# Kernel optimization log

Measured on AMD Instinct MI355X. Metric: run time of the kernel, lower is better.

Reference implementation:

```python
import jax, jax.numpy as jnp
import numpy as np

E = 16      # num_experts
K = 2       # top-k
C = 1280    # capacity = ceil(8192*2/16*1.25)


def setup_inputs() -> dict:
    key = jax.random.key(0)
    ks = jax.random.split(key, 7)
    B, T, D, F, DFF = 4, 2048, 1024, 512, 512
    s = 0.02
    return {
        "hidden_state": jax.random.normal(ks[0], (B, T, D), jnp.float32),
        "router_w": jax.random.normal(ks[1], (D, E), jnp.float32) * s,
        "shared_gate_w": jax.random.normal(ks[2], (D, 1), jnp.float32) * s,
        "w1": jax.random.normal(ks[3], (E, D, F), jnp.float32) * s,
        "w2": jax.random.normal(ks[4], (E, F, D), jnp.float32) * s,
        "sw1": jax.random.normal(ks[5], (D, DFF), jnp.float32) * s,
        "sw2": jax.random.normal(ks[6], (DFF, D), jnp.float32) * s,
    }


def reference(hidden_state, router_w, shared_gate_w, w1, w2, sw1, sw2):
    B, T, D = hidden_state.shape
    N = B * T
    # Router: softmax over expert logits + shared sigmoid gate
    logits = jnp.einsum("btd,de->bte", hidden_state, router_w)
    scores = jax.nn.softmax(logits, axis=-1)                      # [B,T,E]
    g_shared = jax.nn.sigmoid(jnp.einsum("btd,do->bto", hidden_state, shared_gate_w))

    topk_vals, topk_idx = jax.lax.top_k(scores, K)                # [B,T,K]
    x = hidden_state.reshape(N, D)
    token_for_route = jnp.repeat(jnp.arange(N), K)                # [N*K]
    expert_for_route = topk_idx.reshape(-1)                       # [N*K]
    gate_for_route = topk_vals.reshape(-1)                        # [N*K]

    # Stable sort by expert (jnp.argsort is stable)
    order = jnp.argsort(expert_for_route)
    expert_sorted = expert_for_route[order]
    token_sorted = token_for_route[order]
    gate_sorted = gate_for_route[order]
    x_sorted = x[token_sorted]                                    # [N*K, D]

    counts = jnp.bincount(expert_sorted, length=E)
    starts = jnp.cumsum(counts) - counts
    r = jnp.arange(N * K)
    positions = r - starts[expert_sorted]                         # slot within expert
    keep = (positions < C) & (gate_sorted != 0)
    p_idx = jnp.clip(positions, 0, C - 1)

    # Scatter kept tokens into fixed-capacity buffers; dropped routes go to dummy row E
    e_safe = jnp.where(keep, expert_sorted, E)
    p_safe = jnp.where(keep, p_idx, 0)
    buf = jnp.zeros((E + 1, C, D), x.dtype).at[e_safe, p_safe].set(
        jnp.where(keep[:, None], x_sorted, 0.0)
    )
    expert_inputs = buf[:E]                                       # [E,C,D]

    # Batched expert FFN (exact GELU, matching torch default)
    h = jax.nn.gelu(jnp.einsum("ech,ehf->ecf", expert_inputs, w1), approximate=False)
    expert_outputs = jnp.einsum("ecf,efh->ech", h, w2)            # [E,C,D]

    gate_eff = jnp.where(keep, gate_sorted, 0.0)
    y_sorted = expert_outputs[expert_sorted, p_idx] * gate_eff[:, None]

    # Combine: scatter-add back to tokens
    y_out = jnp.zeros((N, D), x.dtype).at[token_sorted].add(y_sorted).reshape(B, T, D)

    # Shared expert path
    shared_out = (jax.nn.gelu(x @ sw1, approximate=False) @ sw2).reshape(B, T, D)
    y_out = y_out + g_shared * shared_out

    # Stats (no attention_mask path)
    load_counts = jnp.bincount(expert_for_route, length=E)
    load = load_counts / (load_counts.sum() + 1e-12)
    importance = scores.mean(axis=(0, 1))
    return (y_out, importance, load)
```

## Files before the change

kernel.cpp:

```cpp
#include <hip/hip_runtime.h>
#include <hip/hip_bf16.h>
#include <math.h>

#define N_TOK 8192
#define DIM 1024
#define NEXP 16
#define CAP 1280
#define FDIM 512
#define NROUTE (N_TOK * 2)
#define NCHUNK 64
#define ECAP (NEXP * CAP)
#define TOTROW (ECAP + N_TOK)

typedef __hip_bfloat16 bf16;
typedef unsigned short ushort_t;
typedef __attribute__((ext_vector_type(8))) short bf16x8;
typedef __attribute__((ext_vector_type(4))) float f32x4;

__device__ __forceinline__ float gelu_fast(float x) {
    float u = 1.5957691216057308f * (x + 0.044715f * x * x * x);
    return x / (1.f + __expf(-u));
}

__device__ __forceinline__ float bf2f(unsigned short u) {
    union { float f; unsigned int i; } v; v.i = ((unsigned int)u) << 16; return v.f;
}

__device__ __forceinline__ unsigned short f2b(float f) {
    union { __hip_bfloat16 h; unsigned short u; } v;
    v.h = __float2bfloat16(f);
    return v.u;
}

__device__ __forceinline__ void gload16(const void* g, void* l) {
    __builtin_amdgcn_global_load_lds(
        (const __attribute__((address_space(1))) unsigned int*)g,
        (__attribute__((address_space(3))) unsigned int*)l,
        16, 0, 0);
}

__device__ __forceinline__ int swz_addr16(int r, int q) {
    return ((r >> 1) << 3) + ((r & 1) << 2) + (q ^ ((r >> 1) & 3));
}

__global__ __launch_bounds__(256) void gather_x_kernel(
    const ushort_t* __restrict__ x_bf, const int* __restrict__ slot_token,
    const int* __restrict__ counts_cap, ushort_t* __restrict__ xg)
{
    int row = blockIdx.x;
    int e = row / CAP;
    int pos = row - e * CAP;
    int tok = (pos < counts_cap[e]) ? slot_token[row] : 0;
    if ((unsigned)tok >= N_TOK) tok = 0;
    int c = threadIdx.x * 4;
    ushort4 v = *reinterpret_cast<const ushort4*>(x_bf + (size_t)tok * DIM + c);
    *reinterpret_cast<ushort4*>(xg + (size_t)row * DIM + c) = v;
}

#define PREP_RTR_BLOCKS 1024
#define PREP_NWG (PREP_RTR_BLOCKS + 1088)
__global__ __launch_bounds__(256) void prep_kernel(
    const float* __restrict__ x, const float* __restrict__ rw,
    const float* __restrict__ sgw,
    const float* __restrict__ w1, const float* __restrict__ w2,
    const float* __restrict__ sw1, const float* __restrict__ sw2,
    float* __restrict__ scores,
    int* __restrict__ topk_idx,
    float* __restrict__ topk_val,
    float* __restrict__ g_shared,
    ushort_t* __restrict__ x_bf,
    ushort_t* __restrict__ w1t, ushort_t* __restrict__ w2t,
    ushort_t* __restrict__ sw1t, ushort_t* __restrict__ sw2t)
{
    __shared__ union {
        ushort_t tileB[128][130];
        struct {
            float xl[8][1028];
            float racc[4][8][4][4];
            float g[4][8];
        } r;
    } sm;

    if (blockIdx.x < PREP_RTR_BLOCKS) {
        int tid = threadIdx.x;
        int w = tid >> 6;
        int lane = tid & 63;
        int tok0 = blockIdx.x * 8;

        {
            int dq = w * 256 + lane * 4;
            float4 gv = *reinterpret_cast<const float4*>(sgw + dq);
#pragma unroll
            for (int tt = 0; tt < 8; ++tt) {
                const float* xr = x + (size_t)(tok0 + tt) * DIM + dq;
                float4 xv = *reinterpret_cast<const float4*>(xr);
                *reinterpret_cast<float4*>(&sm.r.xl[tt][dq]) = xv;
                ushort4 o;
                o.x = f2b(xv.x); o.y = f2b(xv.y); o.z = f2b(xv.z); o.w = f2b(xv.w);
                *reinterpret_cast<ushort4*>(x_bf + (size_t)(tok0 + tt) * DIM + dq) = o;
                float dg = xv.x * gv.x + xv.y * gv.y + xv.z * gv.z + xv.w * gv.w;
#pragma unroll
                for (int m = 1; m < 64; m <<= 1) dg += __shfl_xor(dg, m, 64);
                if (lane == 0) sm.r.g[w][tt] = dg;
            }
        }
        __syncthreads();

        int tok = lane >> 3;
        int dup = (lane >> 2) & 1;
        int e4 = lane & 3;
        {
            int base_d = w * 256 + dup * 128;
            const float* rwb = rw + (size_t)base_d * NEXP + e4 * 4;
            float4 a0 = {0,0,0,0}, a1 = {0,0,0,0}, a2 = {0,0,0,0}, a3 = {0,0,0,0};
#pragma unroll 4
            for (int i = 0; i < 32; ++i) {
                float4 xv = *reinterpret_cast<const float4*>(&sm.r.xl[tok][base_d + i * 4]);
                const float* rp = rwb + (size_t)i * 4 * NEXP;
                float4 w0 = *reinterpret_cast<const float4*>(rp);
                float4 w1v = *reinterpret_cast<const float4*>(rp + NEXP);
                float4 w2v = *reinterpret_cast<const float4*>(rp + 2 * NEXP);
                float4 w3v = *reinterpret_cast<const float4*>(rp + 3 * NEXP);
                a0.x += xv.x * w0.x;  a0.y += xv.x * w0.y;  a0.z += xv.x * w0.z;  a0.w += xv.x * w0.w;
                a1.x += xv.y * w1v.x; a1.y += xv.y * w1v.y; a1.z += xv.y * w1v.z; a1.w += xv.y * w1v.w;
                a2.x += xv.z * w2v.x; a2.y += xv.z * w2v.y; a2.z += xv.z * w2v.z; a2.w += xv.z * w2v.w;
                a3.x += xv.w * w3v.x; a3.y += xv.w * w3v.y; a3.z += xv.w * w3v.z; a3.w += xv.w * w3v.w;
            }
            float s0 = (a0.x + a1.x) + (a2.x + a3.x);
            float s1 = (a0.y + a1.y) + (a2.y + a3.y);
            float s2 = (a0.z + a1.z) + (a2.z + a3.z);
            float s3 = (a0.w + a1.w) + (a2.w + a3.w);
            s0 += __shfl_xor(s0, 4, 64);
            s1 += __shfl_xor(s1, 4, 64);
            s2 += __shfl_xor(s2, 4, 64);
            s3 += __shfl_xor(s3, 4, 64);
            if (dup == 0) {
                sm.r.racc[w][tok][e4][0] = s0;
                sm.r.racc[w][tok][e4][1] = s1;
                sm.r.racc[w][tok][e4][2] = s2;
                sm.r.racc[w][tok][e4][3] = s3;
            }
        }
        __syncthreads();

        if (tid >= 32) return;
        int tk = tid >> 2;
        int eq = tid & 3;
        int token = tok0 + tk;
        float L0 = sm.r.racc[0][tk][eq][0] + sm.r.racc[1][tk][eq][0]
                 + sm.r.racc[2][tk][eq][0] + sm.r.racc[3][tk][eq][0];
        float L1 = sm.r.racc[0][tk][eq][1] + sm.r.racc[1][tk][eq][1]
                 + sm.r.racc[2][tk][eq][1] + sm.r.racc[3][tk][eq][1];
        float L2 = sm.r.racc[0][tk][eq][2] + sm.r.racc[1][tk][eq][2]
                 + sm.r.racc[2][tk][eq][2] + sm.r.racc[3][tk][eq][2];
        float L3 = sm.r.racc[0][tk][eq][3] + sm.r.racc[1][tk][eq][3]
                 + sm.r.racc[2][tk][eq][3] + sm.r.racc[3][tk][eq][3];

        float mx = fmaxf(fmaxf(L0, L1), fmaxf(L2, L3));
        mx = fmaxf(mx, __shfl_xor(mx, 1, 4));
        mx = fmaxf(mx, __shfl_xor(mx, 2, 4));
        float P0 = expf(L0 - mx), P1 = expf(L1 - mx);
        float P2 = expf(L2 - mx), P3 = expf(L3 - mx);
        float s = (P0 + P1) + (P2 + P3);
        s += __shfl_xor(s, 1, 4);
        s += __shfl_xor(s, 2, 4);
        float inv = 1.f / s;
        P0 *= inv; P1 *= inv; P2 *= inv; P3 *= inv;

        float4 Pv = {P0, P1, P2, P3};
        *reinterpret_cast<float4*>(scores + (size_t)token * NEXP + eq * 4) = Pv;

        int base = eq * 4;
        float v = P0; int idx = base;
        if (P1 > v) { v = P1; idx = base + 1; }
        if (P2 > v) { v = P2; idx = base + 2; }
        if (P3 > v) { v = P3; idx = base + 3; }
#pragma unroll
        for (int m = 1; m < 4; m <<= 1) {
            float vo = __shfl_xor(v, m, 4);
            int io = __shfl_xor(idx, m, 4);
            if (vo > v || (vo == v && io < idx)) { v = vo; idx = io; }
        }
        int i0 = idx; float v0 = v;
        float q0 = (base + 0 == i0) ? -1.f : P0;
        float q1 = (base + 1 == i0) ? -1.f : P1;
        float q2 = (base + 2 == i0) ? -1.f : P2;
        float q3 = (base + 3 == i0) ? -1.f : P3;
        v = q0; idx = base;
        if (q1 > v) { v = q1; idx = base + 1; }
        if (q2 > v) { v = q2; idx = base + 2; }
        if (q3 > v) { v = q3; idx = base + 3; }
#pragma unroll
        for (int m = 1; m < 4; m <<= 1) {
            float vo = __shfl_xor(v, m, 4);
            int io = __shfl_xor(idx, m, 4);
            if (vo > v || (vo == v && io < idx)) { v = vo; idx = io; }
        }
        if (eq == 0) {
            topk_idx[2 * token] = i0; topk_idx[2 * token + 1] = idx;
            topk_val[2 * token] = v0; topk_val[2 * token + 1] = v;
            float ag = (sm.r.g[0][tk] + sm.r.g[1][tk]) + (sm.r.g[2][tk] + sm.r.g[3][tk]);
            g_shared[token] = 1.f / (1.f + expf(-ag));
        }
        return;
    }

    int bx = blockIdx.x - PREP_RTR_BLOCKS;
    const float* src; ushort_t* dst; int K, N, kt, nt;
    if (bx < 512) {
        int e = bx >> 5, r = bx & 31;
        K = 1024; N = 512; kt = r >> 2; nt = r & 3;
        src = w1 + (size_t)e * K * N; dst = w1t + (size_t)e * K * N;
    } else if (bx < 1024) {
        int b2 = bx - 512, e = b2 >> 5, r = b2 & 31;
        K = 512; N = 1024; kt = r >> 3; nt = r & 7;
        src = w2 + (size_t)e * K * N; dst = w2t + (size_t)e * K * N;
    } else if (bx < 1056) {
        int r = bx - 1024;
        K = 1024; N = 512; kt = r >> 2; nt = r & 3;
        src = sw1; dst = sw1t;
    } else {
        int r = bx - 1056;
        K = 512; N = 1024; kt = r >> 3; nt = r & 7;
        src = sw2; dst = sw2t;
    }
    int t = threadIdx.x;
#pragma unroll 4
    for (int i = 0; i < 16; ++i) {
        int u = t + 256 * i;
        int r = u >> 5;
        int c4 = (u & 31) * 4;
        float4 v = *reinterpret_cast<const float4*>(
            src + (size_t)(kt * 128 + r) * N + nt * 128 + c4);
        sm.tileB[c4 + 0][r] = f2b(v.x);
        sm.tileB[c4 + 1][r] = f2b(v.y);
        sm.tileB[c4 + 2][r] = f2b(v.z);
        sm.tileB[c4 + 3][r] = f2b(v.w);
    }
    __syncthreads();
#pragma unroll 4
    for (int i2 = 0; i2 < 8; ++i2) {
        int u = t + 256 * i2;
        int n = u >> 4;
        int kc = (u & 15) * 8;
        bf16x8 o;
#pragma unroll
        for (int j = 0; j < 8; ++j) o[j] = (short)sm.tileB[n][kc + j];
        *reinterpret_cast<bf16x8*>(dst + (size_t)(nt * 128 + n) * K + kt * 128 + kc) = o;
    }
}

__global__ __launch_bounds__(256) void hist_kernel(
    const int* __restrict__ topk_idx, int* __restrict__ chunk_hist)
{
    __shared__ int h[NEXP];
    int tid = threadIdx.x;
    if (tid < NEXP) h[tid] = 0;
    __syncthreads();
    int r = blockIdx.x * 256 + tid;
    atomicAdd(&h[topk_idx[r]], 1);
    __syncthreads();
    if (tid < NEXP) chunk_hist[blockIdx.x * NEXP + tid] = h[tid];
}

__global__ __launch_bounds__(64) void scan_kernel(
    const int* __restrict__ chunk_hist, int* __restrict__ chunk_off,
    int* __restrict__ counts_cap, float* __restrict__ out_tail)
{
    int e = threadIdx.x;
    if (e >= NEXP) return;
    int run = 0;
    for (int b = 0; b < NCHUNK; ++b) {
        chunk_off[b * NEXP + e] = run;
        run += chunk_hist[b * NEXP + e];
    }
    counts_cap[e] = run < CAP ? run : CAP;
    out_tail[NEXP + e] = (float)((double)run / 16384.0);
}

__global__ __launch_bounds__(256) void assign_kernel(
    const int* __restrict__ topk_idx, const float* __restrict__ topk_val,
    const int* __restrict__ chunk_off,
    int* __restrict__ route_slot, int* __restrict__ slot_token)
{
    __shared__ int wave_cnt[4][NEXP];
    int tid = threadIdx.x;
    int lane = tid & 63;
    int w = tid >> 6;
    int r = blockIdx.x * 256 + tid;
    int e = topk_idx[r];
    float gate = topk_val[r];
    int rank_w = 0;
#pragma unroll
    for (int e16 = 0; e16 < NEXP; ++e16) {
        unsigned long long bal = __ballot(e == e16);
        if (e == e16) rank_w = __popcll(bal & ((1ull << lane) - 1ull));
        if (lane == 0) wave_cnt[w][e16] = __popcll(bal);
    }
    __syncthreads();
    int rank = rank_w;
#pragma unroll
    for (int w2 = 0; w2 < 3; ++w2)
        if (w2 < w) rank += wave_cnt[w2][e];
    int pos = chunk_off[blockIdx.x * NEXP + e] + rank;
    int slot = -1;
    if (pos < CAP && gate != 0.f) {
        slot = e * CAP + pos;
        slot_token[slot] = r >> 1;
    }
    route_slot[r] = slot;
}

__global__ __launch_bounds__(256) void importance_kernel(
    const float* __restrict__ scores, float* __restrict__ out_tail)
{
    __shared__ float red[256];
    int e = blockIdx.x;
    float s = 0.f;
    for (int t = threadIdx.x; t < N_TOK; t += 256) s += scores[t * NEXP + e];
    red[threadIdx.x] = s;
    __syncthreads();
    for (int st = 128; st > 0; st >>= 1) {
        if (threadIdx.x < st) red[threadIdx.x] += red[threadIdx.x + st];
        __syncthreads();
    }
    if (threadIdx.x == 0) out_tail[e] = red[0] / (float)N_TOK;
}

#define G1_GX (NEXP * 5 + N_TOK / 256)
#define G1_NWG (G1_GX * (FDIM / 128))
__global__ __launch_bounds__(512) void gemm1_mfma(
    const ushort_t* __restrict__ xg,
    const ushort_t* __restrict__ x_bf,
    const ushort_t* __restrict__ w1t,
    const ushort_t* __restrict__ sw1t,
    const int* __restrict__ counts_cap,
    ushort_t* __restrict__ h_buf)
{
    __shared__ ushort_t As[3][256 * 32];
    __shared__ ushort_t Bs[3][128 * 32];

    int flat = blockIdx.x;
    int wg = (flat & 7) * (G1_NWG / 8) + (flat >> 3);
    int by = wg & 3;
    int bxg = wg >> 2;

    int g, rb;
    if (bxg < NEXP * 5) { g = bxg / 5; rb = bxg % 5; }
    else { g = NEXP; rb = bxg - NEXP * 5; }
    int Mg = (g < NEXP) ? counts_cap[g] : N_TOK;
    int m0 = rb * 256;
    if (m0 >= Mg) return;
    const ushort_t* Arows = (g < NEXP) ? (xg + ((size_t)g * CAP + m0) * DIM)
                                       : (x_bf + (size_t)m0 * DIM);
    const ushort_t* Bt = (g < NEXP) ? (w1t + (size_t)g * DIM * FDIM) : sw1t;
    int n0 = by * 128;
    int t = threadIdx.x;

    const ushort_t* asrc[2];
    const ushort_t* bsrc;
#pragma unroll
    for (int i = 0; i < 2; ++i) {
        int s = t + i * 512;
        int lr = ((s >> 3) << 1) | ((s >> 2) & 1);
        int qq = (s & 3) ^ ((s >> 3) & 3);
        asrc[i] = Arows + (size_t)lr * DIM + qq * 8;
    }
    {
        int s = t;
        int lr = ((s >> 3) << 1) | ((s >> 2) & 1);
        int qq = (s & 3) ^ ((s >> 3) & 3);
        bsrc = Bt + (size_t)(n0 + lr) * DIM + qq * 8;
    }

    int lane = t & 63;
    int w = t >> 6;
    int wm = (w & 3) * 64, wn = (w >> 2) * 64;
    int l15 = lane & 15, q = lane >> 4;

    int aoff[4], boff[4];
#pragma unroll
    for (int m = 0; m < 4; ++m) aoff[m] = swz_addr16(wm + m * 16 + l15, q) << 3;
#pragma unroll
    for (int n = 0; n < 4; ++n) boff[n] = swz_addr16(wn + n * 16 + l15, q) << 3;

    f32x4 acc[4][4];
#pragma unroll
    for (int m = 0; m < 4; ++m)
#pragma unroll
        for (int n = 0; n < 4; ++n) acc[m][n] = (f32x4){0.f, 0.f, 0.f, 0.f};

    auto STAGE = [&](int buf, int koff) {
        gload16(asrc[0] + koff, &As[buf][t * 8]);
        gload16(asrc[1] + koff, &As[buf][t * 8 + 4096]);
        gload16(bsrc + koff, &Bs[buf][t * 8]);
    };

    const int NSTEP = DIM / 32;
    STAGE(0, 0);
    STAGE(1, 32);
    asm volatile("s_waitcnt vmcnt(3)" ::: "memory");
    __builtin_amdgcn_s_barrier();
    asm volatile("" ::: "memory");

    int cur = 0, b2 = 2;
    for (int kt = 0; kt < NSTEP; ++kt) {
        if (kt + 2 < NSTEP) STAGE(b2, (kt + 2) * 32);
        const ushort_t* asb = &As[cur][0];
        const ushort_t* bsb = &Bs[cur][0];
        bf16x8 af[4], bfr[4];
#pragma unroll
        for (int m = 0; m < 4; ++m)
            af[m] = *reinterpret_cast<const bf16x8*>(asb + aoff[m]);
#pragma unroll
        for (int n = 0; n < 4; ++n)
            bfr[n] = *reinterpret_cast<const bf16x8*>(bsb + boff[n]);
        __builtin_amdgcn_s_setprio(1);
#pragma unroll
        for (int m = 0; m < 4; ++m)
#pragma unroll
            for (int n = 0; n < 4; ++n)
                acc[m][n] = __builtin_amdgcn_mfma_f32_16x16x32_bf16(
                    af[m], bfr[n], acc[m][n], 0, 0, 0);
        __builtin_amdgcn_s_setprio(0);
        if (kt + 1 < NSTEP) {
            if (kt + 2 < NSTEP) asm volatile("s_waitcnt vmcnt(3)" ::: "memory");
            else                asm volatile("s_waitcnt vmcnt(0)" ::: "memory");
            __builtin_amdgcn_s_barrier();
            asm volatile("" ::: "memory");
        }
        cur = (cur == 2) ? 0 : cur + 1;
        b2  = (b2 == 2) ? 0 : b2 + 1;
    }

    size_t obase = ((g < NEXP) ? (size_t)g * CAP : (size_t)ECAP) + m0;
#pragma unroll
    for (int m = 0; m < 4; ++m) {
#pragma unroll
        for (int r = 0; r < 4; ++r) {
            int grow = wm + m * 16 + q * 4 + r;
            ushort_t* orow = h_buf + (obase + grow) * FDIM + n0 + wn + l15;
#pragma unroll
            for (int n = 0; n < 4; ++n)
                orow[n * 16] = f2b(gelu_fast(acc[m][n][r]));
        }
    }
}

#define G2_NWG (G1_GX * (DIM / 128))
__global__ __launch_bounds__(512) void gemm2_mfma(
    const ushort_t* __restrict__ h_buf,
    const ushort_t* __restrict__ w2t,
    const ushort_t* __restrict__ sw2t,
    const int* __restrict__ counts_cap,
    const float* __restrict__ g_shared,
    ushort_t* __restrict__ out_buf,
    ushort_t* __restrict__ sh_out)
{
    __shared__ ushort_t As[2][256 * 32];
    __shared__ ushort_t Bs[2][128 * 32];

    int flat = blockIdx.x;
    int wg = (flat & 7) * (G2_NWG / 8) + (flat >> 3);
    int by = wg & 7;
    int bxg = wg >> 3;

    int g, rb;
    if (bxg < NEXP * 5) { g = bxg / 5; rb = bxg % 5; }
    else { g = NEXP; rb = bxg - NEXP * 5; }
    int Mg = (g < NEXP) ? counts_cap[g] : N_TOK;
    int m0 = rb * 256;
    if (m0 >= Mg) return;
    size_t abase = ((g < NEXP) ? (size_t)g * CAP : (size_t)ECAP) + m0;
    const ushort_t* Bt = (g < NEXP) ? (w2t + (size_t)g * FDIM * DIM) : sw2t;
    int n0 = by * 128;
    int t = threadIdx.x;

    const ushort_t* asrc[2];
    const ushort_t* bsrc;
#pragma unroll
    for (int i = 0; i < 2; ++i) {
        int s = t + i * 512;
        int lr = ((s >> 3) << 1) | ((s >> 2) & 1);
        int qq = (s & 3) ^ ((s >> 3) & 3);
        asrc[i] = h_buf + (abase + lr) * FDIM + qq * 8;
    }
    {
        int s = t;
        int lr = ((s >> 3) << 1) | ((s >> 2) & 1);
        int qq = (s & 3) ^ ((s >> 3) & 3);
        bsrc = Bt + (size_t)(n0 + lr) * FDIM + qq * 8;
    }

    int lane = t & 63;
    int w = t >> 6;
    int wm = (w & 3) * 64, wn = (w >> 2) * 64;
    int l15 = lane & 15, q = lane >> 4;

    int aoff[4], boff[4];
#pragma unroll
    for (int m = 0; m < 4; ++m) aoff[m] = swz_addr16(wm + m * 16 + l15, q) << 3;
#pragma unroll
    for (int n = 0; n < 4; ++n) boff[n] = swz_addr16(wn + n * 16 + l15, q) << 3;

    f32x4 acc[4][4];
#pragma unroll
    for (int m = 0; m < 4; ++m)
#pragma unroll
        for (int n = 0; n < 4; ++n) acc[m][n] = (f32x4){0.f, 0.f, 0.f, 0.f};

    auto STAGE = [&](int buf, int koff) {
        gload16(asrc[0] + koff, &As[buf][t * 8]);
        gload16(asrc[1] + koff, &As[buf][t * 8 + 4096]);
        gload16(bsrc + koff, &Bs[buf][t * 8]);
    };

    const int NSTEP = FDIM / 32;
    STAGE(0, 0);
    __syncthreads();

    int cur = 0;
    for (int kt = 0; kt < NSTEP; ++kt) {
        if (kt + 1 < NSTEP) STAGE(cur ^ 1, (kt + 1) * 32);
        const ushort_t* asb = &As[cur][0];
        const ushort_t* bsb = &Bs[cur][0];
        bf16x8 af[4], bfr[4];
#pragma unroll
        for (int m = 0; m < 4; ++m)
            af[m] = *reinterpret_cast<const bf16x8*>(asb + aoff[m]);
#pragma unroll
        for (int n = 0; n < 4; ++n)
            bfr[n] = *reinterpret_cast<const bf16x8*>(bsb + boff[n]);
        __builtin_amdgcn_s_setprio(1);
#pragma unroll
        for (int m = 0; m < 4; ++m)
#pragma unroll
            for (int n = 0; n < 4; ++n)
                acc[m][n] = __builtin_amdgcn_mfma_f32_16x16x32_bf16(
                    af[m], bfr[n], acc[m][n], 0, 0, 0);
        __builtin_amdgcn_s_setprio(0);
        __syncthreads();
        cur ^= 1;
    }

    if (g < NEXP) {
#pragma unroll
        for (int m = 0; m < 4; ++m) {
#pragma unroll
            for (int r = 0; r < 4; ++r) {
                int grow = wm + m * 16 + q * 4 + r;
                ushort_t* orow = out_buf + (abase + grow) * DIM + n0 + wn + l15;
#pragma unroll
                for (int n = 0; n < 4; ++n)
                    orow[n * 16] = f2b(acc[m][n][r]);
            }
        }
    } else {
#pragma unroll
        for (int m = 0; m < 4; ++m) {
#pragma unroll
            for (int r = 0; r < 4; ++r) {
                int tok = m0 + wm + m * 16 + q * 4 + r;
                float gs = g_shared[tok];
                ushort_t* orow = sh_out + (size_t)tok * DIM + n0 + wn + l15;
#pragma unroll
                for (int n = 0; n < 4; ++n)
                    orow[n * 16] = f2b(gs * acc[m][n][r]);
            }
        }
    }
}

__global__ __launch_bounds__(256) void combine_kernel(
    const ushort_t* __restrict__ out_buf, const ushort_t* __restrict__ sh_out,
    const int* __restrict__ route_slot, const float* __restrict__ topk_val,
    float* __restrict__ y)
{
    int token = blockIdx.x;
    int c = threadIdx.x * 4;
    ushort4 sv = *reinterpret_cast<const ushort4*>(sh_out + (size_t)token * DIM + c);
    float y0 = bf2f(sv.x), y1 = bf2f(sv.y), y2 = bf2f(sv.z), y3 = bf2f(sv.w);
#pragma unroll
    for (int k = 0; k < 2; ++k) {
        int s = route_slot[2 * token + k];
        if (s >= 0) {
            float gate = topk_val[2 * token + k];
            ushort4 rv = *reinterpret_cast<const ushort4*>(out_buf + (size_t)s * DIM + c);
            y0 += gate * bf2f(rv.x); y1 += gate * bf2f(rv.y);
            y2 += gate * bf2f(rv.z); y3 += gate * bf2f(rv.w);
        }
    }
    float4 o; o.x = y0; o.y = y1; o.z = y2; o.w = y3;
    *reinterpret_cast<float4*>(y + (size_t)token * DIM + c) = o;
}

extern "C" void kernel_launch(void* const* d_in, const int* in_sizes, int n_in,
                              void* d_out, int out_size, void* d_ws, size_t ws_size,
                              hipStream_t stream) {
    const float* x   = (const float*)d_in[0];
    const float* rw  = (const float*)d_in[1];
    const float* sgw = (const float*)d_in[2];
    const float* w1  = (const float*)d_in[3];
    const float* w2  = (const float*)d_in[4];
    const float* sw1 = (const float*)d_in[5];
    const float* sw2 = (const float*)d_in[6];
    float* y = (float*)d_out;
    float* out_tail = y + (size_t)N_TOK * DIM;

    size_t off = 0;
    char* wsb = (char*)d_ws;
    auto alloc = [&](size_t bytes) -> void* {
        void* p = wsb + off;
        off += (bytes + 255) & ~(size_t)255;
        return p;
    };
    float*    scores     = (float*)alloc((size_t)N_TOK * NEXP * 4);
    int*      topk_idx   = (int*)alloc((size_t)NROUTE * 4);
    float*    topk_val   = (float*)alloc((size_t)NROUTE * 4);
    float*    g_shared   = (float*)alloc((size_t)N_TOK * 4);
    int*      chunk_hist = (int*)alloc((size_t)NCHUNK * NEXP * 4);
    int*      chunk_off  = (int*)alloc((size_t)NCHUNK * NEXP * 4);
    int*      counts_cap = (int*)alloc((size_t)NEXP * 4);
    int*      route_slot = (int*)alloc((size_t)NROUTE * 4);
    int*      slot_token = (int*)alloc((size_t)ECAP * 4);
    char*     xg_union   = (char*)alloc((size_t)ECAP * DIM * 2);
    ushort_t* xg         = (ushort_t*)xg_union;
    ushort_t* out_buf    = (ushort_t*)xg_union;
    ushort_t* x_bf       = (ushort_t*)alloc((size_t)N_TOK * DIM * 2);
    ushort_t* sh_out     = x_bf;
    ushort_t* w1t        = (ushort_t*)alloc((size_t)NEXP * DIM * FDIM * 2);
    ushort_t* w2t        = (ushort_t*)alloc((size_t)NEXP * DIM * FDIM * 2);
    ushort_t* sw1t       = (ushort_t*)alloc((size_t)DIM * FDIM * 2);
    ushort_t* sw2t       = (ushort_t*)alloc((size_t)DIM * FDIM * 2);
    ushort_t* h_buf      = (ushort_t*)alloc((size_t)TOTROW * FDIM * 2);
    (void)ws_size; (void)in_sizes; (void)n_in; (void)out_size;

    prep_kernel<<<PREP_NWG, 256, 0, stream>>>(
        x, rw, sgw, w1, w2, sw1, sw2,
        scores, topk_idx, topk_val, g_shared, x_bf, w1t, w2t, sw1t, sw2t);
    hist_kernel<<<NCHUNK, 256, 0, stream>>>(topk_idx, chunk_hist);
    scan_kernel<<<1, 64, 0, stream>>>(chunk_hist, chunk_off, counts_cap, out_tail);
    assign_kernel<<<NCHUNK, 256, 0, stream>>>(topk_idx, topk_val, chunk_off, route_slot, slot_token);
    importance_kernel<<<NEXP, 256, 0, stream>>>(scores, out_tail);
    gather_x_kernel<<<ECAP, 256, 0, stream>>>(x_bf, slot_token, counts_cap, xg);

    gemm1_mfma<<<G1_NWG, 512, 0, stream>>>(xg, x_bf, w1t, sw1t, counts_cap, h_buf);
    gemm2_mfma<<<G2_NWG, 512, 0, stream>>>(h_buf, w2t, sw2t, counts_cap, g_shared, out_buf, sh_out);

    combine_kernel<<<N_TOK, 256, 0, stream>>>(out_buf, sh_out, route_slot, topk_val, y);
}
```

Measured before the change: 167.0 us.

## Fuse token gather into expert GEMM1 A-tile loads via slot_token indirection

Removes the separate gather kernel that copied routed token rows from x_bf into a per-expert capacity buffer. gemm1 now resolves each A row's token index from slot_token and loads straight from x_bf. This avoids writing and re-reading a roughly 40 MB intermediate and drops one launch, at the cost of scattered row addresses in the GEMM's global-to-LDS loads. The transpose tile padding in prep_kernel also changes from 130 to 129 columns, which alters the LDS bank mapping.

After: 153.2 us. 1.09x faster.

```diff
diff --git a/kernel.cpp b/kernel.cpp
--- a/kernel.cpp
+++ b/kernel.cpp
@@ -41,20 +41,6 @@
 
 __device__ __forceinline__ int swz_addr16(int r, int q) {
     return ((r >> 1) << 3) + ((r & 1) << 2) + (q ^ ((r >> 1) & 3));
-}
-
-__global__ __launch_bounds__(256) void gather_x_kernel(
-    const ushort_t* __restrict__ x_bf, const int* __restrict__ slot_token,
-    const int* __restrict__ counts_cap, ushort_t* __restrict__ xg)
-{
-    int row = blockIdx.x;
-    int e = row / CAP;
-    int pos = row - e * CAP;
-    int tok = (pos < counts_cap[e]) ? slot_token[row] : 0;
-    if ((unsigned)tok >= N_TOK) tok = 0;
-    int c = threadIdx.x * 4;
-    ushort4 v = *reinterpret_cast<const ushort4*>(x_bf + (size_t)tok * DIM + c);
-    *reinterpret_cast<ushort4*>(xg + (size_t)row * DIM + c) = v;
 }
 
 #define PREP_RTR_BLOCKS 1024
@@ -73,7 +59,7 @@
     ushort_t* __restrict__ sw1t, ushort_t* __restrict__ sw2t)
 {
     __shared__ union {
-        ushort_t tileB[128][130];
+        ushort_t tileB[128][129];
         struct {
             float xl[8][1028];
             float racc[4][8][4][4];
@@ -330,10 +316,10 @@
 #define G1_GX (NEXP * 5 + N_TOK / 256)
 #define G1_NWG (G1_GX * (FDIM / 128))
 __global__ __launch_bounds__(512) void gemm1_mfma(
-    const ushort_t* __restrict__ xg,
     const ushort_t* __restrict__ x_bf,
     const ushort_t* __restrict__ w1t,
     const ushort_t* __restrict__ sw1t,
+    const int* __restrict__ slot_token,
     const int* __restrict__ counts_cap,
     ushort_t* __restrict__ h_buf)
 {
@@ -351,8 +337,6 @@
     int Mg = (g < NEXP) ? counts_cap[g] : N_TOK;
     int m0 = rb * 256;
     if (m0 >= Mg) return;
-    const ushort_t* Arows = (g < NEXP) ? (xg + ((size_t)g * CAP + m0) * DIM)
-                                       : (x_bf + (size_t)m0 * DIM);
     const ushort_t* Bt = (g < NEXP) ? (w1t + (size_t)g * DIM * FDIM) : sw1t;
     int n0 = by * 128;
     int t = threadIdx.x;
@@ -364,7 +348,16 @@
         int s = t + i * 512;
         int lr = ((s >> 3) << 1) | ((s >> 2) & 1);
         int qq = (s & 3) ^ ((s >> 3) & 3);
-        asrc[i] = Arows + (size_t)lr * DIM + qq * 8;
+        int row = m0 + lr;
+        const ushort_t* base;
+        if (g < NEXP) {
+            int tok = (row < Mg) ? slot_token[g * CAP + row] : 0;
+            if ((unsigned)tok >= N_TOK) tok = 0;
+            base = x_bf + (size_t)tok * DIM;
+        } else {
+            base = x_bf + (size_t)row * DIM;
+        }
+        asrc[i] = base + qq * 8;
     }
     {
         int s = t;
@@ -623,9 +616,7 @@
     int*      counts_cap = (int*)alloc((size_t)NEXP * 4);
     int*      route_slot = (int*)alloc((size_t)NROUTE * 4);
     int*      slot_token = (int*)alloc((size_t)ECAP * 4);
-    char*     xg_union   = (char*)alloc((size_t)ECAP * DIM * 2);
-    ushort_t* xg         = (ushort_t*)xg_union;
-    ushort_t* out_buf    = (ushort_t*)xg_union;
+    ushort_t* out_buf    = (ushort_t*)alloc((size_t)ECAP * DIM * 2);
     ushort_t* x_bf       = (ushort_t*)alloc((size_t)N_TOK * DIM * 2);
     ushort_t* sh_out     = x_bf;
     ushort_t* w1t        = (ushort_t*)alloc((size_t)NEXP * DIM * FDIM * 2);
@@ -642,9 +633,8 @@
     scan_kernel<<<1, 64, 0, stream>>>(chunk_hist, chunk_off, counts_cap, out_tail);
     assign_kernel<<<NCHUNK, 256, 0, stream>>>(topk_idx, topk_val, chunk_off, route_slot, slot_token);
     importance_kernel<<<NEXP, 256, 0, stream>>>(scores, out_tail);
-    gather_x_kernel<<<ECAP, 256, 0, stream>>>(x_bf, slot_token, counts_cap, xg);
-
-    gemm1_mfma<<<G1_NWG, 512, 0, stream>>>(xg, x_bf, w1t, sw1t, counts_cap, h_buf);
+
+    gemm1_mfma<<<G1_NWG, 512, 0, stream>>>(x_bf, w1t, sw1t, slot_token, counts_cap, h_buf);
     gemm2_mfma<<<G2_NWG, 512, 0, stream>>>(h_buf, w2t, sw2t, counts_cap, g_shared, out_buf, sh_out);
 
     combine_kernel<<<N_TOK, 256, 0, stream>>>(out_buf, sh_out, route_slot, topk_val, y);
```
